# Optimization experiments

Hardware: AMD Instinct MI355X
Metric: run time of the kernel (lower is better)

The kernel has to match this reference:

```python
import jax, jax.numpy as jnp
import numpy as np

B, T, D, M, N = 32, 24, 32, 32, 32
H = 32           # hidden_dim (must equal D due to .view in the torch code)
C = M * N        # number of independent per-cell LSTMs
K = 3            # conv kernel size, padding = K // 2


def setup_inputs() -> dict:
    key = jax.random.key(0)
    ks = jax.random.split(key, 7)
    s = 1.0 / np.sqrt(H)  # torch nn.LSTM default init scale
    return {
        "x": jax.random.normal(ks[0], (B, T, D, M, N), jnp.float32),
        "W_ih": jax.random.uniform(ks[1], (C, 4 * H, D), jnp.float32, -s, s),
        "W_hh": jax.random.uniform(ks[2], (C, 4 * H, H), jnp.float32, -s, s),
        "b_ih": jax.random.uniform(ks[3], (C, 4 * H), jnp.float32, -s, s),
        "b_hh": jax.random.uniform(ks[4], (C, 4 * H), jnp.float32, -s, s),
        "conv_w": jax.random.normal(ks[5], (1, H, K, K), jnp.float32) * 0.05,
        "conv_b": jax.random.normal(ks[6], (1,), jnp.float32) * 0.05,
    }


def _spatial_lstm(x, W_ih, W_hh, b_ih, b_hh):
    # x: (B,T,D,M,N) -> per-cell sequences (T,C,B,D)
    xf = x.reshape(B, T, D, C).transpose(1, 3, 0, 2)
    bias = (b_ih + b_hh)[:, None, :]  # (C,1,4H)

    def step(carry, xt):
        h, c = carry  # (C,B,H)
        g = (jnp.einsum('cbd,cgd->cbg', xt, W_ih)
             + jnp.einsum('cbh,cgh->cbg', h, W_hh) + bias)
        i, f, gg, o = jnp.split(g, 4, axis=-1)  # torch gate order i,f,g,o
        c = jax.nn.sigmoid(f) * c + jax.nn.sigmoid(i) * jnp.tanh(gg)
        h = jax.nn.sigmoid(o) * jnp.tanh(c)
        return (h, c), h

    h0 = jnp.zeros((C, B, H), x.dtype)
    _, hs = jax.lax.scan(step, (h0, h0), xf)  # hs: (T,C,B,H)
    # stack over cells, view back to grid: (B,T,H,M,N)
    return hs.transpose(2, 0, 3, 1).reshape(B, T, H, M, N)


def reference(x, W_ih, W_hh, b_ih, b_hh, conv_w, conv_b):
    spatial = _spatial_lstm(x, W_ih, W_hh, b_ih, b_hh)  # (B,T,H,M,N)
    y = jax.lax.conv_general_dilated(
        spatial.reshape(B * T, H, M, N), conv_w,
        window_strides=(1, 1), padding=[(K // 2, K // 2)] * 2,
        dimension_numbers=('NCHW', 'OIHW', 'NCHW'))
    y = y + conv_b[None, :, None, None]
    return jax.nn.sigmoid(y).reshape(B, T, -1, M, N)


if __name__ == "__main__":
    out = reference(**setup_inputs())
    print(out.shape)
```

## Files before the change

### kernel.cpp

```cpp
#include <hip/hip_runtime.h>

#define Bn 32
#define Tn 24
#define Dn 32
#define Hn 32
#define Cn 1024
#define DC (Dn*Cn)
#define TDC (Tn*Dn*Cn)
#define MP 34
#define PPXN (MP*MP)
#define IMGS (MP*MP*32)
#define SCALE 1.442695041f

typedef __attribute__((ext_vector_type(8))) short bf16x8;
typedef __attribute__((ext_vector_type(4))) float f32x4;

union U8 { unsigned u[4]; int4 i; bf16x8 v; };

__device__ __forceinline__ unsigned cvt_pk(float lo, float hi) {
    unsigned r; asm("v_cvt_pk_bf16_f32 %0, %1, %2" : "=v"(r) : "v"(lo), "v"(hi)); return r;
}
__device__ __forceinline__ float lo16f(unsigned u) { return __builtin_bit_cast(float, u << 16); }
__device__ __forceinline__ float hi16f(unsigned u) { return __builtin_bit_cast(float, u & 0xffff0000u); }
__device__ __forceinline__ float rcp_(float x) { return __builtin_amdgcn_rcpf(x); }
__device__ __forceinline__ float exp2_(float x) { return __builtin_amdgcn_exp2f(x); }

struct __align__(16) LdsL {
    unsigned short Xh[2][2][32][48];
    unsigned short Xl[2][2][32][48];
    float Hf[2][2][32][36];
};

__global__ __launch_bounds__(512)
void zero_halo(unsigned short* __restrict__ sp) {
    int gid = blockIdx.x * 512 + threadIdx.x;
    if (gid >= 3072 * 132) return;
    int plane = gid / 132;
    int r = gid - plane * 132;
    int m, n;
    if (r < 34)       { m = 0;      n = r; }
    else if (r < 68)  { m = 33;     n = r - 34; }
    else if (r < 100) { m = r - 67; n = 0; }
    else              { m = r - 99; n = 33; }
    int4 z = {0, 0, 0, 0};
    *(int4*)(sp + ((size_t)plane * PPXN + m * MP + n) * 8) = z;
}

__global__ __launch_bounds__(256, 3)
void lstm_k4(const float* __restrict__ x,
             const float* __restrict__ Wih,
             const float* __restrict__ Whh,
             const float* __restrict__ bih,
             const float* __restrict__ bhh,
             unsigned short* __restrict__ sp)
{
    __shared__ LdsL lds;
    const int tid  = threadIdx.x;
    const int lane = tid & 63;
    const int wave = tid >> 6;
    const int ci   = wave >> 1;
    const int half = wave & 1;
    const int l16  = lane & 15;
    const int kg   = lane >> 4;
    const int bid  = blockIdx.x;
    const int cellbase = (bid & 7) * 128 + (bid >> 3) * 2;
    const int cell = cellbase + ci;

    U8 wihh[4], wihl[4], whhh[4], whhl[4];
    float biasr[4];
#pragma unroll
    for (int q = 0; q < 4; ++q) {
        const int g = q * 32 + half * 16 + l16;
        const float* wp = Wih + (size_t)cell * 4096 + g * 32 + kg * 8;
        const float* hp = Whh + (size_t)cell * 4096 + g * 32 + kg * 8;
        float wv[8], hv[8];
#pragma unroll
        for (int j = 0; j < 8; ++j) { wv[j] = wp[j] * SCALE; hv[j] = hp[j] * SCALE; }
#pragma unroll
        for (int p = 0; p < 4; ++p) {
            unsigned a = cvt_pk(wv[2*p], wv[2*p+1]);
            wihh[q].u[p] = a;
            wihl[q].u[p] = cvt_pk(wv[2*p] - lo16f(a), wv[2*p+1] - hi16f(a));
            unsigned b = cvt_pk(hv[2*p], hv[2*p+1]);
            whhh[q].u[p] = b;
            whhl[q].u[p] = cvt_pk(hv[2*p] - lo16f(b), hv[2*p+1] - hi16f(b));
        }
        biasr[q] = (bih[cell * 128 + g] + bhh[cell * 128 + g]) * SCALE;
    }

    const int sb = tid >> 3;
    const int d0 = (tid & 7) * 4;
    const float* xg0 = x + (size_t)sb * TDC + (size_t)d0 * Cn + cellbase;

    const int sm = cell >> 5, sn = cell & 31;
    const int ppx = (sm + 1) * MP + (sn + 1);
    unsigned short* spb = sp + ((size_t)(half * 16 + l16) * Tn * 4 + kg) * (PPXN * 8)
                             + (size_t)ppx * 8;

    float hD[8] = {};
    float cst[8] = {};
    float2 nx[4];
#pragma unroll
    for (int k = 0; k < 4; ++k) nx[k] = *(const float2*)(xg0 + k * Cn);

    for (int t = 0; t < Tn; ++t) {
        const int bufi = t & 1;
#pragma unroll
        for (int cc = 0; cc < 2; ++cc) {
            float f0 = cc ? nx[0].y : nx[0].x;
            float f1 = cc ? nx[1].y : nx[1].x;
            float f2 = cc ? nx[2].y : nx[2].x;
            float f3 = cc ? nx[3].y : nx[3].x;
            unsigned a0 = cvt_pk(f0, f1), a1 = cvt_pk(f2, f3);
            float l0 = f0 - lo16f(a0), l1 = f1 - hi16f(a0);
            float l2 = f2 - lo16f(a1), l3 = f3 - hi16f(a1);
            int2 hi2 = {(int)a0, (int)a1};
            int2 lo2 = {(int)cvt_pk(l0, l1), (int)cvt_pk(l2, l3)};
            *(int2*)&lds.Xh[bufi][cc][sb][d0] = hi2;
            *(int2*)&lds.Xl[bufi][cc][sb][d0] = lo2;
        }
#pragma unroll
        for (int i = 0; i < 8; ++i) {
            int mt = i >> 2, r = i & 3;
            lds.Hf[bufi][ci][mt * 16 + kg * 4 + r][half * 16 + l16] = hD[i];
        }
        if (t < Tn - 1) {
#pragma unroll
            for (int k = 0; k < 4; ++k)
                nx[k] = *(const float2*)(xg0 + (size_t)(t + 1) * DC + k * Cn);
        }
        __syncthreads();

        U8 xfh[2], xfl[2];
#pragma unroll
        for (int mt = 0; mt < 2; ++mt) {
            xfh[mt].v = *(const bf16x8*)&lds.Xh[bufi][ci][mt * 16 + l16][kg * 8];
            xfl[mt].v = *(const bf16x8*)&lds.Xl[bufi][ci][mt * 16 + l16][kg * 8];
        }
        U8 hfh[2], hfl[2];
        unsigned sphi[4];
#pragma unroll
        for (int mt = 0; mt < 2; ++mt) {
            const float* hp = &lds.Hf[bufi][ci][mt * 16 + l16][kg * 8];
            float4 ha = *(const float4*)hp;
            float4 hb = *(const float4*)(hp + 4);
            float e0 = ha.x, e1 = ha.y, e2 = ha.z, e3 = ha.w;
            float e4 = hb.x, e5 = hb.y, e6 = hb.z, e7 = hb.w;
            unsigned p0 = cvt_pk(e0, e1), p1 = cvt_pk(e2, e3);
            unsigned p2 = cvt_pk(e4, e5), p3 = cvt_pk(e6, e7);
            hfh[mt].u[0] = p0; hfh[mt].u[1] = p1; hfh[mt].u[2] = p2; hfh[mt].u[3] = p3;
            hfl[mt].u[0] = cvt_pk(e0 - lo16f(p0), e1 - hi16f(p0));
            hfl[mt].u[1] = cvt_pk(e2 - lo16f(p1), e3 - hi16f(p1));
            hfl[mt].u[2] = cvt_pk(e4 - lo16f(p2), e5 - hi16f(p2));
            hfl[mt].u[3] = cvt_pk(e6 - lo16f(p3), e7 - hi16f(p3));
            if (mt == half) { sphi[0] = p0; sphi[1] = p1; sphi[2] = p2; sphi[3] = p3; }
        }
        if (t > 0) {
            int4 sv = {(int)sphi[0], (int)sphi[1], (int)sphi[2], (int)sphi[3]};
            *(int4*)(spb + (size_t)(t - 1) * IMGS) = sv;
        }

        f32x4 acc[2][4];
#pragma unroll
        for (int mt = 0; mt < 2; ++mt)
#pragma unroll
            for (int q = 0; q < 4; ++q) {
                f32x4 a = {biasr[q], biasr[q], biasr[q], biasr[q]};
                a = __builtin_amdgcn_mfma_f32_16x16x32_bf16(xfh[mt].v, wihh[q].v, a, 0, 0, 0);
                a = __builtin_amdgcn_mfma_f32_16x16x32_bf16(xfl[mt].v, wihh[q].v, a, 0, 0, 0);
                a = __builtin_amdgcn_mfma_f32_16x16x32_bf16(xfh[mt].v, wihl[q].v, a, 0, 0, 0);
                a = __builtin_amdgcn_mfma_f32_16x16x32_bf16(hfh[mt].v, whhh[q].v, a, 0, 0, 0);
                a = __builtin_amdgcn_mfma_f32_16x16x32_bf16(hfl[mt].v, whhh[q].v, a, 0, 0, 0);
                a = __builtin_amdgcn_mfma_f32_16x16x32_bf16(hfh[mt].v, whhl[q].v, a, 0, 0, 0);
                acc[mt][q] = a;
            }

#pragma unroll
        for (int mt = 0; mt < 2; ++mt)
#pragma unroll
            for (int r = 0; r < 4; ++r) {
                float gi = acc[mt][0][r], gf = acc[mt][1][r];
                float gg = acc[mt][2][r], go = acc[mt][3][r];
                float ig = rcp_(1.f + exp2_(-gi));
                float fg = rcp_(1.f + exp2_(-gf));
                float gt = 1.f - 2.f * rcp_(1.f + exp2_(gg + gg));
                float og = rcp_(1.f + exp2_(-go));
                float c  = fg * cst[mt * 4 + r] + ig * gt;
                cst[mt * 4 + r] = c;
                float tc = 1.f - 2.f * rcp_(1.f + exp2_((2.f * SCALE) * c));
                hD[mt * 4 + r] = og * tc;
            }
    }

#pragma unroll
    for (int i = 0; i < 8; ++i) {
        int mt = i >> 2, r = i & 3;
        lds.Hf[0][ci][mt * 16 + kg * 4 + r][half * 16 + l16] = hD[i];
    }
    __syncthreads();
    {
        const float* hp = &lds.Hf[0][ci][half * 16 + l16][kg * 8];
        float4 ha = *(const float4*)hp;
        float4 hb = *(const float4*)(hp + 4);
        int4 sv = {(int)cvt_pk(ha.x, ha.y), (int)cvt_pk(ha.z, ha.w),
                   (int)cvt_pk(hb.x, hb.y), (int)cvt_pk(hb.z, hb.w)};
        *(int4*)(spb + (size_t)(Tn - 1) * IMGS) = sv;
    }
}

__global__ __launch_bounds__(512, 4)
void conv_k4(const unsigned short* __restrict__ sp,
             const float* __restrict__ cw,
             const float* __restrict__ cb,
             float* __restrict__ out)
{
    __shared__ float wlds[9][32];
    const int tid = threadIdx.x;
    const int img = blockIdx.x;
    if (tid < 288) wlds[tid >> 5][tid & 31] = cw[(tid & 31) * 9 + (tid >> 5)];
    __syncthreads();
    const float bias = cb[0];
    float acc[2] = {bias, bias};
    int ppx[2];
#pragma unroll
    for (int pk = 0; pk < 2; ++pk) {
        int px = tid + pk * 512;
        ppx[pk] = ((px >> 5) + 1) * MP + (px & 31) + 1;
    }
#pragma unroll
    for (int hc = 0; hc < 4; ++hc) {
        float4 wa[9], wb[9];
#pragma unroll
        for (int tap = 0; tap < 9; ++tap) {
            wa[tap] = *(const float4*)&wlds[tap][hc * 8];
            wb[tap] = *(const float4*)&wlds[tap][hc * 8 + 4];
        }
        const unsigned short* plane = sp + (size_t)(img * 4 + hc) * (PPXN * 8);
#pragma unroll
        for (int pk = 0; pk < 2; ++pk) {
            const unsigned short* base = plane + (size_t)ppx[pk] * 8;
            float a = acc[pk];
#pragma unroll
            for (int dm = -1; dm <= 1; ++dm)
#pragma unroll
                for (int dn = -1; dn <= 1; ++dn) {
                    const int tap = (dm + 1) * 3 + (dn + 1);
                    int4 v = *(const int4*)(base + (dm * MP + dn) * 8);
                    float4 w0 = wa[tap], w1 = wb[tap];
                    a = fmaf(lo16f((unsigned)v.x), w0.x, a);
                    a = fmaf(hi16f((unsigned)v.x), w0.y, a);
                    a = fmaf(lo16f((unsigned)v.y), w0.z, a);
                    a = fmaf(hi16f((unsigned)v.y), w0.w, a);
                    a = fmaf(lo16f((unsigned)v.z), w1.x, a);
                    a = fmaf(hi16f((unsigned)v.z), w1.y, a);
                    a = fmaf(lo16f((unsigned)v.w), w1.z, a);
                    a = fmaf(hi16f((unsigned)v.w), w1.w, a);
                }
            acc[pk] = a;
        }
    }
#pragma unroll
    for (int pk = 0; pk < 2; ++pk)
        out[(size_t)img * 1024 + tid + pk * 512] = rcp_(1.f + exp2_(-SCALE * acc[pk]));
}

extern "C" void kernel_launch(void* const* d_in, const int* in_sizes, int n_in,
                              void* d_out, int out_size, void* d_ws, size_t ws_size,
                              hipStream_t stream) {
    const float* x   = (const float*)d_in[0];
    const float* Wih = (const float*)d_in[1];
    const float* Whh = (const float*)d_in[2];
    const float* bih = (const float*)d_in[3];
    const float* bhh = (const float*)d_in[4];
    const float* cw  = (const float*)d_in[5];
    const float* cb  = (const float*)d_in[6];
    float* out = (float*)d_out;
    unsigned short* sp = (unsigned short*)d_ws;

    zero_halo<<<792, 512, 0, stream>>>(sp);
    lstm_k4<<<512, 256, 0, stream>>>(x, Wih, Whh, bih, bhh, sp);
    conv_k4<<<Bn * Tn, 512, 0, stream>>>(sp, cw, cb, out);
}
```

Baseline: 102.4 us.

## Assign one cell per LSTM block, splitting batch across waves

Each LSTM block now handles a single cell, with its four waves split over batch halves and gate halves, rather than two cells per block with waves split over gate halves. The grid doubles to 1024 blocks and the occupancy hint rises to 4 blocks per CU. Per-wave MFMA and gate work per step is halved, which shortens the serial recurrence critical path. The cost is that per-cell weights are loaded and split into bf16 high/low parts by twice as many waves, and the x loads become scalar rather than float2.

```diff
diff --git a/kernel.cpp b/kernel.cpp
--- a/kernel.cpp
+++ b/kernel.cpp
@@ -26,9 +26,9 @@
 __device__ __forceinline__ float exp2_(float x) { return __builtin_amdgcn_exp2f(x); }
 
 struct __align__(16) LdsL {
-    unsigned short Xh[2][2][32][48];
-    unsigned short Xl[2][2][32][48];
-    float Hf[2][2][32][36];
+    unsigned short Xh[2][32][48];
+    unsigned short Xl[2][32][48];
+    float Hf[2][32][36];
 };
 
 __global__ __launch_bounds__(512)
@@ -46,8 +46,8 @@
     *(int4*)(sp + ((size_t)plane * PPXN + m * MP + n) * 8) = z;
 }
 
-__global__ __launch_bounds__(256, 3)
-void lstm_k4(const float* __restrict__ x,
+__global__ __launch_bounds__(256, 4)
+void lstm_k5(const float* __restrict__ x,
              const float* __restrict__ Wih,
              const float* __restrict__ Whh,
              const float* __restrict__ bih,
@@ -58,19 +58,18 @@
     const int tid  = threadIdx.x;
     const int lane = tid & 63;
     const int wave = tid >> 6;
-    const int ci   = wave >> 1;
-    const int half = wave & 1;
+    const int bh   = wave >> 1;
+    const int gh   = wave & 1;
     const int l16  = lane & 15;
     const int kg   = lane >> 4;
     const int bid  = blockIdx.x;
-    const int cellbase = (bid & 7) * 128 + (bid >> 3) * 2;
-    const int cell = cellbase + ci;
+    const int cell = (bid & 7) * 128 + (bid >> 3);
 
     U8 wihh[4], wihl[4], whhh[4], whhl[4];
     float biasr[4];
 #pragma unroll
     for (int q = 0; q < 4; ++q) {
-        const int g = q * 32 + half * 16 + l16;
+        const int g = q * 32 + gh * 16 + l16;
         const float* wp = Wih + (size_t)cell * 4096 + g * 32 + kg * 8;
         const float* hp = Whh + (size_t)cell * 4096 + g * 32 + kg * 8;
         float wv[8], hv[8];
@@ -90,116 +89,90 @@
 
     const int sb = tid >> 3;
     const int d0 = (tid & 7) * 4;
-    const float* xg0 = x + (size_t)sb * TDC + (size_t)d0 * Cn + cellbase;
+    const float* xg0 = x + (size_t)sb * TDC + (size_t)d0 * Cn + cell;
 
     const int sm = cell >> 5, sn = cell & 31;
     const int ppx = (sm + 1) * MP + (sn + 1);
-    unsigned short* spb = sp + ((size_t)(half * 16 + l16) * Tn * 4 + kg) * (PPXN * 8)
+    unsigned short* spb = sp + ((size_t)(bh * 16 + l16) * Tn * 4 + kg) * (PPXN * 8)
                              + (size_t)ppx * 8;
 
-    float hD[8] = {};
-    float cst[8] = {};
-    float2 nx[4];
-#pragma unroll
-    for (int k = 0; k < 4; ++k) nx[k] = *(const float2*)(xg0 + k * Cn);
+    float hD[4] = {};
+    float cst[4] = {};
+    float nx0 = xg0[0], nx1 = xg0[Cn], nx2 = xg0[2 * Cn], nx3 = xg0[3 * Cn];
 
     for (int t = 0; t < Tn; ++t) {
         const int bufi = t & 1;
-#pragma unroll
-        for (int cc = 0; cc < 2; ++cc) {
-            float f0 = cc ? nx[0].y : nx[0].x;
-            float f1 = cc ? nx[1].y : nx[1].x;
-            float f2 = cc ? nx[2].y : nx[2].x;
-            float f3 = cc ? nx[3].y : nx[3].x;
-            unsigned a0 = cvt_pk(f0, f1), a1 = cvt_pk(f2, f3);
-            float l0 = f0 - lo16f(a0), l1 = f1 - hi16f(a0);
-            float l2 = f2 - lo16f(a1), l3 = f3 - hi16f(a1);
+        {
+            unsigned a0 = cvt_pk(nx0, nx1), a1 = cvt_pk(nx2, nx3);
+            float r0 = nx0 - lo16f(a0), r1 = nx1 - hi16f(a0);
+            float r2 = nx2 - lo16f(a1), r3 = nx3 - hi16f(a1);
             int2 hi2 = {(int)a0, (int)a1};
-            int2 lo2 = {(int)cvt_pk(l0, l1), (int)cvt_pk(l2, l3)};
-            *(int2*)&lds.Xh[bufi][cc][sb][d0] = hi2;
-            *(int2*)&lds.Xl[bufi][cc][sb][d0] = lo2;
-        }
-#pragma unroll
-        for (int i = 0; i < 8; ++i) {
-            int mt = i >> 2, r = i & 3;
-            lds.Hf[bufi][ci][mt * 16 + kg * 4 + r][half * 16 + l16] = hD[i];
-        }
+            int2 lo2 = {(int)cvt_pk(r0, r1), (int)cvt_pk(r2, r3)};
+            *(int2*)&lds.Xh[bufi][sb][d0] = hi2;
+            *(int2*)&lds.Xl[bufi][sb][d0] = lo2;
+        }
+#pragma unroll
+        for (int r = 0; r < 4; ++r)
+            lds.Hf[bufi][bh * 16 + kg * 4 + r][gh * 16 + l16] = hD[r];
         if (t < Tn - 1) {
-#pragma unroll
-            for (int k = 0; k < 4; ++k)
-                nx[k] = *(const float2*)(xg0 + (size_t)(t + 1) * DC + k * Cn);
+            const float* xg = xg0 + (size_t)(t + 1) * DC;
+            nx0 = xg[0]; nx1 = xg[Cn]; nx2 = xg[2 * Cn]; nx3 = xg[3 * Cn];
         }
         __syncthreads();
 
-        U8 xfh[2], xfl[2];
-#pragma unroll
-        for (int mt = 0; mt < 2; ++mt) {
-            xfh[mt].v = *(const bf16x8*)&lds.Xh[bufi][ci][mt * 16 + l16][kg * 8];
-            xfl[mt].v = *(const bf16x8*)&lds.Xl[bufi][ci][mt * 16 + l16][kg * 8];
-        }
-        U8 hfh[2], hfl[2];
-        unsigned sphi[4];
-#pragma unroll
-        for (int mt = 0; mt < 2; ++mt) {
-            const float* hp = &lds.Hf[bufi][ci][mt * 16 + l16][kg * 8];
-            float4 ha = *(const float4*)hp;
-            float4 hb = *(const float4*)(hp + 4);
-            float e0 = ha.x, e1 = ha.y, e2 = ha.z, e3 = ha.w;
-            float e4 = hb.x, e5 = hb.y, e6 = hb.z, e7 = hb.w;
-            unsigned p0 = cvt_pk(e0, e1), p1 = cvt_pk(e2, e3);
-            unsigned p2 = cvt_pk(e4, e5), p3 = cvt_pk(e6, e7);
-            hfh[mt].u[0] = p0; hfh[mt].u[1] = p1; hfh[mt].u[2] = p2; hfh[mt].u[3] = p3;
-            hfl[mt].u[0] = cvt_pk(e0 - lo16f(p0), e1 - hi16f(p0));
-            hfl[mt].u[1] = cvt_pk(e2 - lo16f(p1), e3 - hi16f(p1));
-            hfl[mt].u[2] = cvt_pk(e4 - lo16f(p2), e5 - hi16f(p2));
-            hfl[mt].u[3] = cvt_pk(e6 - lo16f(p3), e7 - hi16f(p3));
-            if (mt == half) { sphi[0] = p0; sphi[1] = p1; sphi[2] = p2; sphi[3] = p3; }
-        }
-        if (t > 0) {
-            int4 sv = {(int)sphi[0], (int)sphi[1], (int)sphi[2], (int)sphi[3]};
+        U8 xfh, xfl;
+        xfh.v = *(const bf16x8*)&lds.Xh[bufi][bh * 16 + l16][kg * 8];
+        xfl.v = *(const bf16x8*)&lds.Xl[bufi][bh * 16 + l16][kg * 8];
+        U8 hfh, hfl;
+        const float* hp = &lds.Hf[bufi][bh * 16 + l16][kg * 8];
+        float4 ha = *(const float4*)hp;
+        float4 hb = *(const float4*)(hp + 4);
+        unsigned p0 = cvt_pk(ha.x, ha.y), p1 = cvt_pk(ha.z, ha.w);
+        unsigned p2 = cvt_pk(hb.x, hb.y), p3 = cvt_pk(hb.z, hb.w);
+        hfh.u[0] = p0; hfh.u[1] = p1; hfh.u[2] = p2; hfh.u[3] = p3;
+        hfl.u[0] = cvt_pk(ha.x - lo16f(p0), ha.y - hi16f(p0));
+        hfl.u[1] = cvt_pk(ha.z - lo16f(p1), ha.w - hi16f(p1));
+        hfl.u[2] = cvt_pk(hb.x - lo16f(p2), hb.y - hi16f(p2));
+        hfl.u[3] = cvt_pk(hb.z - lo16f(p3), hb.w - hi16f(p3));
+        if (gh == 0 && t > 0) {
+            int4 sv = {(int)p0, (int)p1, (int)p2, (int)p3};
             *(int4*)(spb + (size_t)(t - 1) * IMGS) = sv;
         }
 
-        f32x4 acc[2][4];
-#pragma unroll
-        for (int mt = 0; mt < 2; ++mt)
-#pragma unroll
-            for (int q = 0; q < 4; ++q) {
-                f32x4 a = {biasr[q], biasr[q], biasr[q], biasr[q]};
-                a = __builtin_amdgcn_mfma_f32_16x16x32_bf16(xfh[mt].v, wihh[q].v, a, 0, 0, 0);
-                a = __builtin_amdgcn_mfma_f32_16x16x32_bf16(xfl[mt].v, wihh[q].v, a, 0, 0, 0);
-                a = __builtin_amdgcn_mfma_f32_16x16x32_bf16(xfh[mt].v, wihl[q].v, a, 0, 0, 0);
-                a = __builtin_amdgcn_mfma_f32_16x16x32_bf16(hfh[mt].v, whhh[q].v, a, 0, 0, 0);
-                a = __builtin_amdgcn_mfma_f32_16x16x32_bf16(hfl[mt].v, whhh[q].v, a, 0, 0, 0);
-                a = __builtin_amdgcn_mfma_f32_16x16x32_bf16(hfh[mt].v, whhl[q].v, a, 0, 0, 0);
-                acc[mt][q] = a;
-            }
-
-#pragma unroll
-        for (int mt = 0; mt < 2; ++mt)
-#pragma unroll
-            for (int r = 0; r < 4; ++r) {
-                float gi = acc[mt][0][r], gf = acc[mt][1][r];
-                float gg = acc[mt][2][r], go = acc[mt][3][r];
-                float ig = rcp_(1.f + exp2_(-gi));
-                float fg = rcp_(1.f + exp2_(-gf));
-                float gt = 1.f - 2.f * rcp_(1.f + exp2_(gg + gg));
-                float og = rcp_(1.f + exp2_(-go));
-                float c  = fg * cst[mt * 4 + r] + ig * gt;
-                cst[mt * 4 + r] = c;
-                float tc = 1.f - 2.f * rcp_(1.f + exp2_((2.f * SCALE) * c));
-                hD[mt * 4 + r] = og * tc;
-            }
-    }
-
-#pragma unroll
-    for (int i = 0; i < 8; ++i) {
-        int mt = i >> 2, r = i & 3;
-        lds.Hf[0][ci][mt * 16 + kg * 4 + r][half * 16 + l16] = hD[i];
-    }
+        f32x4 acc[4];
+#pragma unroll
+        for (int q = 0; q < 4; ++q) {
+            f32x4 a = {biasr[q], biasr[q], biasr[q], biasr[q]};
+            a = __builtin_amdgcn_mfma_f32_16x16x32_bf16(xfh.v, wihh[q].v, a, 0, 0, 0);
+            a = __builtin_amdgcn_mfma_f32_16x16x32_bf16(xfl.v, wihh[q].v, a, 0, 0, 0);
+            a = __builtin_amdgcn_mfma_f32_16x16x32_bf16(xfh.v, wihl[q].v, a, 0, 0, 0);
+            a = __builtin_amdgcn_mfma_f32_16x16x32_bf16(hfh.v, whhh[q].v, a, 0, 0, 0);
+            a = __builtin_amdgcn_mfma_f32_16x16x32_bf16(hfl.v, whhh[q].v, a, 0, 0, 0);
+            a = __builtin_amdgcn_mfma_f32_16x16x32_bf16(hfh.v, whhl[q].v, a, 0, 0, 0);
+            acc[q] = a;
+        }
+
+#pragma unroll
+        for (int r = 0; r < 4; ++r) {
+            float gi = acc[0][r], gf = acc[1][r];
+            float gg = acc[2][r], go = acc[3][r];
+            float ig = rcp_(1.f + exp2_(-gi));
+            float fg = rcp_(1.f + exp2_(-gf));
+            float gt = 1.f - 2.f * rcp_(1.f + exp2_(gg + gg));
+            float og = rcp_(1.f + exp2_(-go));
+            float c  = fg * cst[r] + ig * gt;
+            cst[r] = c;
+            float tc = 1.f - 2.f * rcp_(1.f + exp2_((2.f * SCALE) * c));
+            hD[r] = og * tc;
+        }
+    }
+
+#pragma unroll
+    for (int r = 0; r < 4; ++r)
+        lds.Hf[0][bh * 16 + kg * 4 + r][gh * 16 + l16] = hD[r];
     __syncthreads();
-    {
-        const float* hp = &lds.Hf[0][ci][half * 16 + l16][kg * 8];
+    if (gh == 0) {
+        const float* hp = &lds.Hf[0][bh * 16 + l16][kg * 8];
         float4 ha = *(const float4*)hp;
         float4 hb = *(const float4*)(hp + 4);
         int4 sv = {(int)cvt_pk(ha.x, ha.y), (int)cvt_pk(ha.z, ha.w),
@@ -278,6 +251,6 @@
     unsigned short* sp = (unsigned short*)d_ws;
 
     zero_halo<<<792, 512, 0, stream>>>(sp);
-    lstm_k4<<<512, 256, 0, stream>>>(x, Wih, Whh, bih, bhh, sp);
+    lstm_k5<<<1024, 256, 0, stream>>>(x, Wih, Whh, bih, bhh, sp);
     conv_k4<<<Bn * Tn, 512, 0, stream>>>(sp, cw, cb, out);
 }
```

After: 165.1 us. 1.61x slower.
